# Kernel tuning notes

Measured on AMD Instinct MI355X. Metric: run time of the kernel, lower is better.

The kernel has to match this reference:

```python
import jax, jax.numpy as jnp
import numpy as np

Q_BITS = 8
GELU_A = -0.2888
GELU_B = -1.769
INV_SQRT2 = 0.7071067811865476


def _ste_round(x):
    # straight-through round (identity grad)
    return x + jax.lax.stop_gradient(jnp.round(x) - x)


def fake_quant_weight(w):
    # per-tensor symmetric int8 fake quant
    qmax = 2.0 ** (Q_BITS - 1) - 1.0  # 127
    s = jnp.maximum(jnp.max(jnp.abs(w)), 1e-8) / qmax
    q = jnp.clip(_ste_round(w / s), -qmax - 1.0, qmax)
    return q * s


def fake_quant_act(x):
    # per-tensor asymmetric uint8 fake quant
    levels = 2.0 ** Q_BITS - 1.0  # 255
    xmin = jax.lax.stop_gradient(jnp.min(x))
    xmax = jax.lax.stop_gradient(jnp.max(x))
    s = jnp.maximum(xmax - xmin, 1e-8) / levels
    zp = jnp.round(-xmin / s)
    q = jnp.clip(_ste_round(x / s) + zp, 0.0, levels)
    return (q - zp) * s


def int_gelu(x):
    # I-BERT polynomial GELU: gelu(x) = x * 0.5 * (1 + L(x/sqrt(2)))
    # L(t) = sign(t) * (a * (clip(|t|, 0, -b) + b)^2 + 1)
    t = x * INV_SQRT2
    at = jnp.minimum(jnp.abs(t), -GELU_B)
    L = jnp.sign(t) * (GELU_A * (at + GELU_B) ** 2 + 1.0)
    return x * 0.5 * (1.0 + L)


def setup_inputs() -> dict:
    key = jax.random.key(0)
    k = jax.random.split(key, 5)
    B, S, D, H = 64, 197, 768, 3072
    x = jax.random.normal(k[0], (B, S, D), dtype=jnp.float32)
    w1 = jax.random.normal(k[1], (H, D), dtype=jnp.float32) * (1.0 / np.sqrt(D))
    b1 = jax.random.normal(k[2], (H,), dtype=jnp.float32) * 0.02
    w2 = jax.random.normal(k[3], (D, H), dtype=jnp.float32) * (1.0 / np.sqrt(H))
    b2 = jax.random.normal(k[4], (D,), dtype=jnp.float32) * 0.02
    return {"x": x, "w1": w1, "b1": b1, "w2": w2, "b2": b2}


def reference(x, w1, b1, w2, b2):
    # QuantLinear 1: fake-quant act + weight, then GEMM
    xq = fake_quant_act(x)
    h = jnp.einsum('bsd,hd->bsh', xq, fake_quant_weight(w1)) + b1
    # IntGELU (dropout is identity in eval)
    g = int_gelu(h)
    # QuantLinear 2
    gq = fake_quant_act(g)
    out = jnp.einsum('bsh,dh->bsd', gq, fake_quant_weight(w2)) + b2
    return out
```

## Files before the change

kernel.cpp:

```cpp
#include <hip/hip_runtime.h>
#include <stdint.h>
#include <stddef.h>

typedef int v4i __attribute__((ext_vector_type(4)));

#define GELU_A   (-0.2888f)
#define GELU_B   (-1.769f)
#define INV_SQRT2 0.70710678118654752440f

__device__ __forceinline__ unsigned enc_f(float f){
  unsigned u = __float_as_uint(f);
  return (u & 0x80000000u) ? ~u : (u | 0x80000000u);
}
__device__ __forceinline__ float dec_f(unsigned e){
  unsigned u = (e & 0x80000000u) ? (e & 0x7FFFFFFFu) : ~e;
  return __uint_as_float(u);
}

__device__ __forceinline__ float int_gelu_f(float x){
  float t = x * INV_SQRT2;
  float at = fminf(fabsf(t), 1.769f);
  float u = at + GELU_B;
  float p = GELU_A * (u * u) + 1.0f;
  float L = (t > 0.0f) ? p : ((t < 0.0f) ? -p : 0.0f);
  return x * 0.5f * (1.0f + L);
}

__global__ void init_scalars(unsigned* sc){
  if (threadIdx.x == 0){
    sc[0] = 0xFFFFFFFFu;
    sc[1] = 0u;
    sc[2] = 0u;
    sc[3] = 0u;
    sc[4] = 0xFFFFFFFFu;
    sc[5] = 0u;
  }
}

__global__ __launch_bounds__(256) void reduce_stats(
    const float4* __restrict__ x, int nx4,
    const float4* __restrict__ w1, int n14,
    const float4* __restrict__ w2, int n24,
    unsigned* __restrict__ sc)
{
  __shared__ float ra[256], rb[256];
  const int tid = threadIdx.x;
  const int b = blockIdx.x;
  if (b < 512){
    float lmin = 3.4e38f, lmax = -3.4e38f;
    for (long i = (long)b * 256 + tid; i < nx4; i += 512L * 256L){
      float4 v = x[i];
      lmin = fminf(lmin, fminf(fminf(v.x, v.y), fminf(v.z, v.w)));
      lmax = fmaxf(lmax, fmaxf(fmaxf(v.x, v.y), fmaxf(v.z, v.w)));
    }
    ra[tid] = lmin; rb[tid] = lmax;
    __syncthreads();
    for (int s = 128; s > 0; s >>= 1){
      if (tid < s){ ra[tid] = fminf(ra[tid], ra[tid + s]); rb[tid] = fmaxf(rb[tid], rb[tid + s]); }
      __syncthreads();
    }
    if (tid == 0){
      atomicMin(&sc[0], enc_f(ra[0]));
      atomicMax(&sc[1], enc_f(rb[0]));
    }
  } else {
    const float4* w; int n4; int slot; int bl;
    if (b < 640){ w = w1; n4 = n14; slot = 2; bl = b - 512; }
    else        { w = w2; n4 = n24; slot = 3; bl = b - 640; }
    float la = 0.0f;
    for (long i = (long)bl * 256 + tid; i < n4; i += 128L * 256L){
      float4 v = w[i];
      la = fmaxf(la, fmaxf(fmaxf(fabsf(v.x), fabsf(v.y)), fmaxf(fabsf(v.z), fabsf(v.w))));
    }
    ra[tid] = la;
    __syncthreads();
    for (int s = 128; s > 0; s >>= 1){
      if (tid < s) ra[tid] = fmaxf(ra[tid], ra[tid + s]);
      __syncthreads();
    }
    if (tid == 0) atomicMax(&sc[slot], __float_as_uint(ra[0]));
  }
}

__global__ __launch_bounds__(256) void quant_act(
    const float4* __restrict__ in, unsigned* __restrict__ out, long n4,
    const unsigned* __restrict__ sc, int slot)
{
  const float vmin = dec_f(sc[slot]);
  const float vmax = dec_f(sc[slot + 1]);
  const float s  = fmaxf(vmax - vmin, 1e-8f) / 255.0f;
  const float zp = rintf(-vmin / s);
  const long stride = (long)gridDim.x * blockDim.x;
  for (long i = (long)blockIdx.x * blockDim.x + threadIdx.x; i < n4; i += stride){
    float4 v = in[i];
    int q0 = (int)fminf(fmaxf(rintf(v.x / s) + zp, 0.0f), 255.0f) - 128;
    int q1 = (int)fminf(fmaxf(rintf(v.y / s) + zp, 0.0f), 255.0f) - 128;
    int q2 = (int)fminf(fmaxf(rintf(v.z / s) + zp, 0.0f), 255.0f) - 128;
    int q3 = (int)fminf(fmaxf(rintf(v.w / s) + zp, 0.0f), 255.0f) - 128;
    out[i] = ((unsigned)(q0 & 255)) | ((unsigned)(q1 & 255) << 8) |
             ((unsigned)(q2 & 255) << 16) | ((unsigned)(q3 & 255) << 24);
  }
}

__global__ __launch_bounds__(256) void quant_w(
    const float* __restrict__ w1, const float* __restrict__ w2,
    int8_t* __restrict__ qw1, int8_t* __restrict__ qw2,
    int* __restrict__ rs1, int* __restrict__ rs2,
    const unsigned* __restrict__ sc, int n1, int k1, int k2)
{
  __shared__ int red[256];
  const int b = blockIdx.x, tid = threadIdx.x;
  const float* w; int8_t* q; int* rs; int K; int n; float s;
  if (b < n1){ w = w1; q = qw1; rs = rs1; K = k1; n = b;
               s = fmaxf(__uint_as_float(sc[2]), 1e-8f) / 127.0f; }
  else       { w = w2; q = qw2; rs = rs2; K = k2; n = b - n1;
               s = fmaxf(__uint_as_float(sc[3]), 1e-8f) / 127.0f; }
  int sum = 0;
  for (int k = tid; k < K; k += 256){
    float v = w[(size_t)n * K + k];
    float qf = fminf(fmaxf(rintf(v / s), -128.0f), 127.0f);
    int qi = (int)qf;
    q[(size_t)n * K + k] = (int8_t)qi;
    sum += qi;
  }
  red[tid] = sum;
  __syncthreads();
  for (int st = 128; st > 0; st >>= 1){
    if (tid < st) red[tid] += red[tid + st];
    __syncthreads();
  }
  if (tid == 0) rs[n] = red[0];
}

template<int MODE>
__global__ __launch_bounds__(256) void gemm_i8(
    const int8_t* __restrict__ A, const int8_t* __restrict__ Bm,
    const int* __restrict__ rowsum, const float* __restrict__ bias,
    void* __restrict__ Cout, int M, int N, int K,
    unsigned* __restrict__ sc)
{
  __shared__ __align__(16) int8_t ldsA[128 * 80];
  __shared__ __align__(16) int8_t ldsB[128 * 80];
  __shared__ float redA[256];
  __shared__ float redB[256];

  const int tid  = threadIdx.x;
  const int n0   = blockIdx.x * 128;
  const int m0   = blockIdx.y * 128;
  const int lane = tid & 63;
  const int wave = tid >> 6;
  const int m16  = lane & 15;
  const int quad = lane >> 4;
  const int wm   = (wave & 1) * 64;
  const int wn   = (wave >> 1) * 64;

  const int sr  = tid >> 2;
  const int scn = tid & 3;
  int mg0 = m0 + sr;      if (mg0 >= M) mg0 = M - 1;
  int mg1 = m0 + sr + 64; if (mg1 >= M) mg1 = M - 1;
  const size_t aoff0 = (size_t)mg0 * K + scn * 16;
  const size_t aoff1 = (size_t)mg1 * K + scn * 16;
  const size_t boff0 = (size_t)(n0 + sr) * K + scn * 16;
  const size_t boff1 = (size_t)(n0 + sr + 64) * K + scn * 16;
  int8_t* wA0 = ldsA + sr * 80 + scn * 16;
  int8_t* wA1 = ldsA + (sr + 64) * 80 + scn * 16;
  int8_t* wB0 = ldsB + sr * 80 + scn * 16;
  int8_t* wB1 = ldsB + (sr + 64) * 80 + scn * 16;

  v4i acc[4][4] = {};

  for (int k0 = 0; k0 < K; k0 += 64){
    uint4 a0 = *(const uint4*)(A + aoff0 + k0);
    uint4 a1 = *(const uint4*)(A + aoff1 + k0);
    uint4 b0 = *(const uint4*)(Bm + boff0 + k0);
    uint4 b1 = *(const uint4*)(Bm + boff1 + k0);
    __syncthreads();
    *(uint4*)wA0 = a0; *(uint4*)wA1 = a1;
    *(uint4*)wB0 = b0; *(uint4*)wB1 = b1;
    __syncthreads();
    v4i af[4], bf[4];
#pragma unroll
    for (int i = 0; i < 4; i++){
      af[i] = *(const v4i*)(ldsA + (wm + i * 16 + m16) * 80 + quad * 16);
      bf[i] = *(const v4i*)(ldsB + (wn + i * 16 + m16) * 80 + quad * 16);
    }
#pragma unroll
    for (int i = 0; i < 4; i++)
#pragma unroll
      for (int j = 0; j < 4; j++)
        acc[i][j] = __builtin_amdgcn_mfma_i32_16x16x64_i8(af[i], bf[j], acc[i][j], 0, 0, 0);
  }

  float s_h, off_h;
  if constexpr (MODE == 1){
    float gmin = dec_f(sc[4]), gmax = dec_f(sc[5]);
    float sg = fmaxf(gmax - gmin, 1e-8f) / 255.0f;
    float zp = rintf(-gmin / sg);
    float sw = fmaxf(__uint_as_float(sc[3]), 1e-8f) / 127.0f;
    s_h = sg * sw; off_h = 128.0f - zp;
  } else {
    float xmin = dec_f(sc[0]), xmax = dec_f(sc[1]);
    float sx = fmaxf(xmax - xmin, 1e-8f) / 255.0f;
    float zp = rintf(-xmin / sx);
    float sw = fmaxf(__uint_as_float(sc[2]), 1e-8f) / 127.0f;
    s_h = sx * sw; off_h = 128.0f - zp;
  }
  float qs = 1.0f, qzp = 0.0f;
  if constexpr (MODE == 2){
    float gmin = dec_f(sc[4]), gmax = dec_f(sc[5]);
    qs = fmaxf(gmax - gmin, 1e-8f) / 255.0f;
    qzp = rintf(-gmin / qs);
  }

  float lmin = 3.4e38f, lmax = -3.4e38f;
#pragma unroll
  for (int j = 0; j < 4; j++){
    const int n = n0 + wn + j * 16 + m16;
    const float rsv = off_h * (float)rowsum[n];
    const float bv = bias[n];
#pragma unroll
    for (int i = 0; i < 4; i++){
      const int mbase = m0 + wm + i * 16 + quad * 4;
#pragma unroll
      for (int r = 0; r < 4; r++){
        const int m = mbase + r;
        if (m < M){
          float h = s_h * ((float)acc[i][j][r] + rsv) + bv;
          if constexpr (MODE == 0){
            float gv = int_gelu_f(h);
            lmin = fminf(lmin, gv); lmax = fmaxf(lmax, gv);
          } else if constexpr (MODE == 2){
            float gv = int_gelu_f(h);
            float qf = fminf(fmaxf(rintf(gv / qs) + qzp, 0.0f), 255.0f);
            ((int8_t*)Cout)[(size_t)m * N + n] = (int8_t)((int)qf - 128);
          } else {
            ((float*)Cout)[(size_t)m * N + n] = h;
          }
        }
      }
    }
  }

  if constexpr (MODE == 0){
    redA[tid] = lmin; redB[tid] = lmax;
    __syncthreads();
    for (int st = 128; st > 0; st >>= 1){
      if (tid < st){
        redA[tid] = fminf(redA[tid], redA[tid + st]);
        redB[tid] = fmaxf(redB[tid], redB[tid + st]);
      }
      __syncthreads();
    }
    if (tid == 0){
      atomicMin(&sc[4], enc_f(redA[0]));
      atomicMax(&sc[5], enc_f(redB[0]));
    }
  }
}

extern "C" void kernel_launch(void* const* d_in, const int* in_sizes, int n_in,
                              void* d_out, int out_size, void* d_ws, size_t ws_size,
                              hipStream_t stream)
{
  const float* x  = (const float*)d_in[0];
  const float* w1 = (const float*)d_in[1];
  const float* b1 = (const float*)d_in[2];
  const float* w2 = (const float*)d_in[3];
  const float* b2 = (const float*)d_in[4];
  float* out = (float*)d_out;

  const int H = in_sizes[2];
  const int D = in_sizes[4];
  const int M = in_sizes[0] / D;

  char* ws = (char*)d_ws;
  unsigned* sc = (unsigned*)ws;
  size_t off = 256;
  int8_t* qx  = (int8_t*)(ws + off); off += (size_t)M * D;
  int8_t* qw1 = (int8_t*)(ws + off); off += (size_t)H * D;
  int8_t* qw2 = (int8_t*)(ws + off); off += (size_t)D * H;
  int* rs1 = (int*)(ws + off); off += (size_t)H * 4;
  int* rs2 = (int*)(ws + off); off += 4096;
  int8_t* qg  = (int8_t*)(ws + off); off += (size_t)M * H;
  (void)ws_size; (void)n_in; (void)out_size;

  init_scalars<<<dim3(1), dim3(64), 0, stream>>>(sc);

  reduce_stats<<<dim3(768), dim3(256), 0, stream>>>(
      (const float4*)x, M * D / 4,
      (const float4*)w1, H * D / 4,
      (const float4*)w2, D * H / 4, sc);

  quant_act<<<dim3(1024), dim3(256), 0, stream>>>(
      (const float4*)x, (unsigned*)qx, (long)M * D / 4, sc, 0);

  quant_w<<<dim3(H + D), dim3(256), 0, stream>>>(
      w1, w2, qw1, qw2, rs1, rs2, sc, H, D, H);

  gemm_i8<0><<<dim3(H / 128, (M + 127) / 128), dim3(256), 0, stream>>>(
      qx, qw1, rs1, b1, nullptr, M, H, D, sc);

  gemm_i8<2><<<dim3(H / 128, (M + 127) / 128), dim3(256), 0, stream>>>(
      qx, qw1, rs1, b1, qg, M, H, D, sc);

  gemm_i8<1><<<dim3(D / 128, (M + 127) / 128), dim3(256), 0, stream>>>(
      qg, qw2, rs2, b2, out, M, D, H, sc);
}
```

Baseline: 374.7 us.

## Stage B in large K-slabs in LDS and load A fragments directly from global

The int8 MFMA GEMM now loads B in 384-wide K slabs into a padded LDS buffer, so it syncs once per slab instead of once per 64-wide K step. A fragments are read straight from global memory into registers per wave, with no LDS staging. The reduction scratch reuses the B LDS buffer, and launch bounds ask for 3 blocks per CU. The risks are uncoalesced or duplicated global loads for A, since the waves sharing a row band each read it, and the fact that K must be a multiple of 384.

```diff
diff --git a/kernel.cpp b/kernel.cpp
--- a/kernel.cpp
+++ b/kernel.cpp
@@ -133,62 +133,69 @@
 }
 
 template<int MODE>
-__global__ __launch_bounds__(256) void gemm_i8(
+__global__ __launch_bounds__(256, 3) void gemm_i8(
     const int8_t* __restrict__ A, const int8_t* __restrict__ Bm,
     const int* __restrict__ rowsum, const float* __restrict__ bias,
     void* __restrict__ Cout, int M, int N, int K,
     unsigned* __restrict__ sc)
 {
-  __shared__ __align__(16) int8_t ldsA[128 * 80];
-  __shared__ __align__(16) int8_t ldsB[128 * 80];
-  __shared__ float redA[256];
-  __shared__ float redB[256];
+  constexpr int KSLAB = 384;
+  constexpr int LSTR  = 400;
+  __shared__ __align__(16) int8_t ldsB[128 * LSTR];
 
   const int tid  = threadIdx.x;
+  const int lane = tid & 63;
+  const int wave = tid >> 6;
   const int n0   = blockIdx.x * 128;
   const int m0   = blockIdx.y * 128;
-  const int lane = tid & 63;
-  const int wave = tid >> 6;
   const int m16  = lane & 15;
   const int quad = lane >> 4;
   const int wm   = (wave & 1) * 64;
   const int wn   = (wave >> 1) * 64;
 
-  const int sr  = tid >> 2;
-  const int scn = tid & 3;
-  int mg0 = m0 + sr;      if (mg0 >= M) mg0 = M - 1;
-  int mg1 = m0 + sr + 64; if (mg1 >= M) mg1 = M - 1;
-  const size_t aoff0 = (size_t)mg0 * K + scn * 16;
-  const size_t aoff1 = (size_t)mg1 * K + scn * 16;
-  const size_t boff0 = (size_t)(n0 + sr) * K + scn * 16;
-  const size_t boff1 = (size_t)(n0 + sr + 64) * K + scn * 16;
-  int8_t* wA0 = ldsA + sr * 80 + scn * 16;
-  int8_t* wA1 = ldsA + (sr + 64) * 80 + scn * 16;
-  int8_t* wB0 = ldsB + sr * 80 + scn * 16;
-  int8_t* wB1 = ldsB + (sr + 64) * 80 + scn * 16;
+  const int8_t* aptr[4];
+#pragma unroll
+  for (int i = 0; i < 4; i++){
+    int mr = m0 + wm + i * 16 + m16;
+    if (mr >= M) mr = M - 1;
+    aptr[i] = A + (size_t)mr * K + quad * 16;
+  }
 
   v4i acc[4][4] = {};
 
-  for (int k0 = 0; k0 < K; k0 += 64){
-    uint4 a0 = *(const uint4*)(A + aoff0 + k0);
-    uint4 a1 = *(const uint4*)(A + aoff1 + k0);
-    uint4 b0 = *(const uint4*)(Bm + boff0 + k0);
-    uint4 b1 = *(const uint4*)(Bm + boff1 + k0);
-    __syncthreads();
-    *(uint4*)wA0 = a0; *(uint4*)wA1 = a1;
-    *(uint4*)wB0 = b0; *(uint4*)wB1 = b1;
-    __syncthreads();
-    v4i af[4], bf[4];
-#pragma unroll
-    for (int i = 0; i < 4; i++){
-      af[i] = *(const v4i*)(ldsA + (wm + i * 16 + m16) * 80 + quad * 16);
-      bf[i] = *(const v4i*)(ldsB + (wn + i * 16 + m16) * 80 + quad * 16);
-    }
-#pragma unroll
-    for (int i = 0; i < 4; i++)
+  const int nslabs = K / KSLAB;
+  for (int s = 0; s < nslabs; s++){
+    const int ks = s * KSLAB;
+    uint4 breg[12];
+#pragma unroll
+    for (int t = 0; t < 12; t++){
+      int idx = tid + t * 256;
+      int r = idx / 24, c = idx - r * 24;
+      breg[t] = *(const uint4*)(Bm + (size_t)(n0 + r) * K + ks + c * 16);
+    }
+    __syncthreads();
+#pragma unroll
+    for (int t = 0; t < 12; t++){
+      int idx = tid + t * 256;
+      int r = idx / 24, c = idx - r * 24;
+      *(uint4*)(ldsB + r * LSTR + c * 16) = breg[t];
+    }
+    __syncthreads();
+#pragma unroll
+    for (int kk = 0; kk < KSLAB; kk += 64){
+      v4i af[4], bf[4];
 #pragma unroll
       for (int j = 0; j < 4; j++)
-        acc[i][j] = __builtin_amdgcn_mfma_i32_16x16x64_i8(af[i], bf[j], acc[i][j], 0, 0, 0);
+        bf[j] = *(const v4i*)(ldsB + (wn + j * 16 + m16) * LSTR + kk + quad * 16);
+#pragma unroll
+      for (int i = 0; i < 4; i++)
+        af[i] = *(const v4i*)(aptr[i] + ks + kk);
+#pragma unroll
+      for (int i = 0; i < 4; i++)
+#pragma unroll
+        for (int j = 0; j < 4; j++)
+          acc[i][j] = __builtin_amdgcn_mfma_i32_16x16x64_i8(af[i], bf[j], acc[i][j], 0, 0, 0);
+    }
   }
 
   float s_h, off_h;
@@ -242,6 +249,9 @@
   }
 
   if constexpr (MODE == 0){
+    __syncthreads();
+    float* redA = (float*)ldsB;
+    float* redB = ((float*)ldsB) + 256;
     redA[tid] = lmin; redB[tid] = lmax;
     __syncthreads();
     for (int st = 128; st > 0; st >>= 1){
```

New measurement: 648.5 us. +73.1%, slower.
